# Kernel tuning notes

Hardware: AMD Instinct MI355X
Metric: run time of the kernel (lower is better)

Reference implementation:

```python
import jax, jax.numpy as jnp
import numpy as np

BATCH, NUM_BSS, NUM_USERS, M, N = 32, 8, 32, 128, 4
LAGR_ITERS = 8
PSEUDOINV_SVAL_THRESH = 1e-12


def herm(a):
    return 0.5 * (a + jnp.swapaxes(a, -1, -2).conj())


def setup_inputs() -> dict:
    key = jax.random.key(0)
    ks = jax.random.split(key, 7)
    v_re = jax.random.normal(ks[0], (BATCH, NUM_USERS, M, N), jnp.float32)
    v_im = jax.random.normal(ks[1], (BATCH, NUM_USERS, M, N), jnp.float32)
    H_re = jax.random.normal(ks[2], (NUM_BSS, NUM_USERS, N, M), jnp.float32)
    H_im = jax.random.normal(ks[3], (NUM_BSS, NUM_USERS, N, M), jnp.float32)
    noise_pow = jax.random.uniform(ks[4], (BATCH, NUM_USERS), jnp.float32, 0.05, 1.0)
    rweights = jax.random.uniform(ks[5], (BATCH, NUM_USERS), jnp.float32, 0.1, 1.0)
    bss_pow = jnp.ones((BATCH, NUM_BSS), jnp.float32)
    assign = jax.random.randint(ks[6], (NUM_USERS,), 0, NUM_BSS).astype(jnp.int32)
    return {"v_re": v_re, "v_im": v_im, "H_re": H_re, "H_im": H_im,
            "noise_pow": noise_pow, "rweights": rweights, "bss_pow": bss_pow,
            "assign": assign}


def reference(v_re, v_im, H_re, H_im, noise_pow, rweights, bss_pow, assign):
    V = v_re + 1j * v_im          # [B,K,M,N] precoders
    H = H_re + 1j * H_im          # [C,K,N,M] channel BS c -> user k
    K = V.shape[1]
    C = H.shape[0]
    Ndim = V.shape[-1]
    eyeN = jnp.eye(Ndim, dtype=V.dtype)

    # Hg[j, i] = channel from assigned-BS-of-user-j to user i
    Hg = H[assign]                                    # [K,K,N,M]
    # downlink covariance per user i: noise*I + sum_j (H[bs_j,i] V_j)(.)^H
    HV = jnp.einsum('jinm,bjmp->bijnp', Hg, V)        # [B,Ki,Kj,N,N]
    cov = jnp.einsum('bijnp,bijqp->binq', HV, HV.conj())
    cov = herm(cov + noise_pow[..., None, None] * eyeN)
    icov = herm(jnp.linalg.inv(cov))                  # [B,K,N,N]

    idx = jnp.arange(K)
    Hd = Hg[idx, idx]                                 # [K,N,M] direct channels
    HdV = jnp.einsum('knm,bkmp->bknp', Hd, V)         # [B,K,N,N]
    u = jnp.einsum('bknq,bkqp->bknp', icov, HdV)      # receive filters
    w_inv = herm(eyeN - jnp.einsum('bkqn,bkqp->bknp', u.conj(), HdV))
    w = herm(jnp.linalg.inv(w_inv))                   # MSE weights (w_poly=None)
    uwu = herm(jnp.einsum('bknp,bkpq,bkrq->bknr', u, w, u.conj()))
    # v_tilde = H_ii^H u w * rate_weight
    vt = jnp.einsum('knm,bknp,bkpq->bkmq', Hd.conj(), u, w) * rweights[..., None, None]

    # uplink covariance per BS c: sum_k rw_k * H[c,k]^H uwu_k H[c,k]
    ul = herm(jnp.einsum('cknm,bkno,ckop,bk->bcmp', H.conj(), uwu, H, rweights))

    # aux per BS: sum over assigned users of v_tilde v_tilde^H
    Q = jnp.einsum('bkmn,bkpn->bkmp', vt, vt.conj())  # [B,K,M,M]
    aux = jnp.moveaxis(
        jax.ops.segment_sum(jnp.moveaxis(Q, 1, 0), assign, num_segments=C), 0, 1)  # [B,C,M,M]

    lam, E = jnp.linalg.eigh(ul)                      # [B,C,M], [B,C,M,M]
    lam = jnp.maximum(lam, 0.0)
    c = jnp.maximum(jnp.einsum('bcmi,bcmp,bcpi->bci', E.conj(), aux, E).real, 0.0)
    c = c / bss_pow[..., None]

    # solve sum_i c_i/(lam_i+mu)^2 = 1 for mu >= 0 by bisection in [0, sqrt(sum c)]
    hi = jnp.sqrt(jnp.sum(c, -1))
    lo = jnp.zeros_like(hi)
    for _ in range(LAGR_ITERS):
        mid = 0.5 * (lo + hi)
        f = jnp.sum(c / jnp.square(lam + mid[..., None] + 1e-20), -1)
        gt = f > 1.0
        lo = jnp.where(gt, mid, lo)
        hi = jnp.where(gt, hi, mid)
    mu = jnp.maximum(0.5 * (lo + hi), 0.0)            # [B,C]

    # pseudo-inverse of loaded UL covariance via its eigendecomposition
    lam_l = lam + mu[..., None]
    lam_l = jnp.where(lam_l < PSEUDOINV_SVAL_THRESH, 1e12, lam_l)
    inv_aug = herm(jnp.einsum('bcmi,bci,bcni->bcmn', E, 1.0 / lam_l, E.conj()))

    # v update: v_k = inv_aug[assign_k] @ v_tilde_k
    v_out = jnp.einsum('bkmp,bkpn->bkmn', inv_aug[:, assign], vt)  # [B,K,M,N]
    return v_out
```

## Files before the change

kernel.cpp:

```cpp
#include <hip/hip_runtime.h>

#define B_ 32
#define C_ 8
#define K_ 32

__device__ __forceinline__ float2 cmul(float2 a, float2 b) {
  return make_float2(a.x*b.x - a.y*b.y, a.x*b.y + a.y*b.x);
}
__device__ __forceinline__ float2 cmulc(float2 a, float2 b) {
  return make_float2(a.x*b.x + a.y*b.y, a.y*b.x - a.x*b.y);
}
__device__ __forceinline__ float2 cadd(float2 a, float2 b){ return make_float2(a.x+b.x, a.y+b.y); }
__device__ __forceinline__ float2 csub(float2 a, float2 b){ return make_float2(a.x-b.x, a.y-b.y); }
__device__ __forceinline__ int SK(int r){ return r + ((r >> 3) << 1); }

__device__ void herm4_inv(float2 a[4][4], float2 out[4][4]) {
  float idg[4];
  for (int j = 0; j < 4; ++j) {
    float d = sqrtf(fmaxf(a[j][j].x, 1e-30f));
    float id = 1.f / d;
    idg[j] = id;
    a[j][j] = make_float2(d, 0.f);
    for (int r = j+1; r < 4; ++r) { a[r][j].x *= id; a[r][j].y *= id; }
    for (int c = j+1; c < 4; ++c)
      for (int r = c; r < 4; ++r)
        a[r][c] = csub(a[r][c], cmulc(a[r][j], a[c][j]));
  }
  float2 li[4][4];
  for (int j = 0; j < 4; ++j) {
    li[j][j] = make_float2(idg[j], 0.f);
    for (int r = j+1; r < 4; ++r) {
      float2 s = make_float2(0.f, 0.f);
      for (int d = j; d < r; ++d) s = cadd(s, cmul(a[r][d], li[d][j]));
      li[r][j] = make_float2(-s.x*idg[r], -s.y*idg[r]);
    }
  }
  for (int p = 0; p < 4; ++p)
    for (int q = 0; q < 4; ++q) {
      float2 s = make_float2(0.f, 0.f);
      for (int d = (p > q ? p : q); d < 4; ++d)
        s = cadd(s, cmulc(li[d][q], li[d][p]));
      out[p][q] = s;
    }
}

__global__ __launch_bounds__(512, 2) void k_fused(
    const float* __restrict__ v_re, const float* __restrict__ v_im,
    const float* __restrict__ H_re, const float* __restrict__ H_im,
    const float* __restrict__ noise_pow, const float* __restrict__ rweights,
    const float* __restrict__ bss_pow, const int* __restrict__ assign_g,
    void* __restrict__ outp, int omode)
{
  const int t = threadIdx.x;
  const int lane = t & 63, wid = t >> 6;
  const int blk = blockIdx.x;
  const int b = blk >> 3, c = blk & 7;
  const int tm = t >> 4, tp = t & 15;
  const int rbase = tm * 4, cbase = tp * 8;

  __shared__ __align__(16) float2 Arena[4160];
  __shared__ __align__(16) float2 pS[1024];
  __shared__ __align__(16) float2 dBS2[256];
  __shared__ __align__(16) float2 vS[128];
  __shared__ __align__(16) float2 wS[160];
  __shared__ __align__(16) float2 colS[160];
  __shared__ __align__(16) float2 pvS[128];
  __shared__ __align__(16) float2 tauS[128];
  __shared__ float dS[128], eS[128], cpS[128];
  __shared__ float red[8];
  __shared__ int asg[K_], ulist[K_], nc_s;

  float2* Wall = pS;
  float2* uwS  = pS + 512;
  float2* Vs   = Arena;
  float2* Tb   = Arena + 776;
  float2* covS = Arena + 1288;
  float2* HdVS = Arena + 1800;
  float2* Hs   = Arena;
  float2* Ys   = Arena + 520;
  float2* Pd   = Arena;
  float2* Bs   = Arena;

  if (t < K_) asg[t] = assign_g[t];
  if (t == 0) {
    int n2 = 0;
    for (int k = 0; k < K_; ++k) if (assign_g[k] == c) ulist[n2++] = k;
    nc_s = n2;
  }
  {
    const int k = t >> 4, n = (t >> 2) & 3, q = t & 3;
    covS[t] = make_float2((n == q) ? noise_pow[b*K_ + k] : 0.f, 0.f);
  }
  __syncthreads();
  const int nc = nc_s;
  if (nc == 0) return;
  const int cols = 4 * nc;
  const int qmax = (cols + 15) >> 4;
  const int passes = (cols + 31) >> 5;

  {
    const int pn = t >> 2;
    const int qt = t & 3;
    const int kk = pn >> 2, nn = pn & 3;
    const float2* Vq = Vs + qt*2;
    for (int j = 0; j < K_; ++j) {
      const int vb = (b*K_ + j) * 512;
      Vs[(t >> 2)*6 + (t & 3) + (t >> 7)*2] = make_float2(v_re[vb + t], v_im[vb + t]);
      __syncthreads();
      const int hb = ((asg[j]*K_ + kk)*4 + nn) * 128;
      float2 a0 = {0,0}, a1 = {0,0}, a2 = {0,0}, a3 = {0,0};
      for (int m4 = qt*32; m4 < qt*32 + 32; m4 += 4) {
        const float4 hre = *(const float4*)&H_re[hb + m4];
        const float4 him = *(const float4*)&H_im[hb + m4];
        const float hx[4] = {hre.x, hre.y, hre.z, hre.w};
        const float hy[4] = {him.x, him.y, him.z, him.w};
        #pragma unroll
        for (int i = 0; i < 4; ++i) {
          const float4 v01 = *(const float4*)&Vq[(m4 + i)*6];
          const float4 v23 = *(const float4*)&Vq[(m4 + i)*6 + 2];
          a0.x += hx[i]*v01.x - hy[i]*v01.y; a0.y += hx[i]*v01.y + hy[i]*v01.x;
          a1.x += hx[i]*v01.z - hy[i]*v01.w; a1.y += hx[i]*v01.w + hy[i]*v01.z;
          a2.x += hx[i]*v23.x - hy[i]*v23.y; a2.y += hx[i]*v23.y + hy[i]*v23.x;
          a3.x += hx[i]*v23.z - hy[i]*v23.w; a3.y += hx[i]*v23.w + hy[i]*v23.z;
        }
      }
      #pragma unroll
      for (int o = 1; o <= 2; o <<= 1) {
        a0.x += __shfl_xor(a0.x, o, 64); a0.y += __shfl_xor(a0.y, o, 64);
        a1.x += __shfl_xor(a1.x, o, 64); a1.y += __shfl_xor(a1.y, o, 64);
        a2.x += __shfl_xor(a2.x, o, 64); a2.y += __shfl_xor(a2.y, o, 64);
        a3.x += __shfl_xor(a3.x, o, 64); a3.y += __shfl_xor(a3.y, o, 64);
      }
      if (qt == 0) {
        Tb[pn*4 + 0] = a0; Tb[pn*4 + 1] = a1; Tb[pn*4 + 2] = a2; Tb[pn*4 + 3] = a3;
      }
      __syncthreads();
      {
        const int k2 = t >> 4, n2 = (t >> 2) & 3, q2 = t & 3;
        float2 acc = covS[t];
        #pragma unroll
        for (int p = 0; p < 4; ++p)
          acc = cadd(acc, cmulc(Tb[(k2*4 + n2)*4 + p], Tb[(k2*4 + q2)*4 + p]));
        covS[t] = acc;
        if (k2 == j) HdVS[k2*16 + n2*4 + q2] = Tb[(k2*4 + n2)*4 + q2];
      }
      __syncthreads();
    }
  }

  if (t < K_) {
    const int k = t;
    float2 a[4][4], ic[4][4], hv[4][4], u[4][4], wi[4][4], w[4][4], uw[4][4], W[4][4];
    const float rwk = rweights[b*K_ + k];
    for (int r = 0; r < 4; ++r)
      for (int c2 = 0; c2 < 4; ++c2) a[r][c2] = covS[k*16 + r*4 + c2];
    herm4_inv(a, ic);
    for (int r = 0; r < 4; ++r)
      for (int c2 = 0; c2 < 4; ++c2) hv[r][c2] = HdVS[k*16 + r*4 + c2];
    for (int n = 0; n < 4; ++n)
      for (int p = 0; p < 4; ++p) {
        float2 s = {0,0};
        for (int q = 0; q < 4; ++q) s = cadd(s, cmul(ic[n][q], hv[q][p]));
        u[n][p] = s;
      }
    for (int n = 0; n < 4; ++n)
      for (int p = 0; p < 4; ++p) {
        float2 s = make_float2((n == p) ? 1.f : 0.f, 0.f);
        for (int q = 0; q < 4; ++q) s = csub(s, cmulc(hv[q][p], u[q][n]));
        wi[n][p] = s;
      }
    herm4_inv(wi, w);
    for (int n = 0; n < 4; ++n)
      for (int q = 0; q < 4; ++q) {
        float2 s = {0,0};
        for (int p = 0; p < 4; ++p) s = cadd(s, cmul(u[n][p], w[p][q]));
        uw[n][q] = s;
      }
    for (int n = 0; n < 4; ++n)
      for (int r = 0; r < 4; ++r) {
        float2 s = {0,0};
        for (int q = 0; q < 4; ++q) s = cadd(s, cmulc(uw[n][q], u[r][q]));
        W[n][r] = make_float2(s.x * rwk, s.y * rwk);
      }
    for (int n = 0; n < 4; ++n)
      for (int r = n; r < 4; ++r) {
        float2 x1 = W[n][r], x2 = W[r][n];
        float2 hm = make_float2(0.5f*(x1.x + x2.x), 0.5f*(x1.y - x2.y));
        W[n][r] = hm; W[r][n] = make_float2(hm.x, -hm.y);
      }
    for (int idx = 0; idx < 16; ++idx) {
      uwS[k*16 + idx]  = uw[idx >> 2][idx & 3];
      Wall[k*16 + idx] = W[idx >> 2][idx & 3];
    }
  }
  __syncthreads();

  float2 Bv[4][8];
  #pragma unroll
  for (int j = 0; j < 4; ++j)
    #pragma unroll
    for (int q = 0; q < 8; ++q) Bv[j][q] = make_float2(0.f, 0.f);
  float trp = 0.f;
  #pragma unroll
  for (int q = 0; q < 8; ++q) {
    const int col = tp + 16*q;
    const int slot = col >> 2, qn = col & 3;
    if (slot < nc) {
      const int k = ulist[slot];
      const float rwk = rweights[b*K_ + k];
      const int hb = (c*K_ + k) * 512;
      float2 acc0 = {0,0}, acc1 = {0,0}, acc2 = {0,0}, acc3 = {0,0};
      #pragma unroll
      for (int n = 0; n < 4; ++n) {
        const float2 uwv = uwS[k*16 + n*4 + qn];
        const float4 hre = *(const float4*)&H_re[hb + n*128 + rbase];
        const float4 him = *(const float4*)&H_im[hb + n*128 + rbase];
        acc0 = cadd(acc0, cmulc(uwv, make_float2(hre.x, him.x)));
        acc1 = cadd(acc1, cmulc(uwv, make_float2(hre.y, him.y)));
        acc2 = cadd(acc2, cmulc(uwv, make_float2(hre.z, him.z)));
        acc3 = cadd(acc3, cmulc(uwv, make_float2(hre.w, him.w)));
      }
      acc0.x *= rwk; acc0.y *= rwk; acc1.x *= rwk; acc1.y *= rwk;
      acc2.x *= rwk; acc2.y *= rwk; acc3.x *= rwk; acc3.y *= rwk;
      Bv[0][q] = acc0; Bv[1][q] = acc1; Bv[2][q] = acc2; Bv[3][q] = acc3;
      trp += acc0.x*acc0.x + acc0.y*acc0.y + acc1.x*acc1.x + acc1.y*acc1.y
           + acc2.x*acc2.x + acc2.y*acc2.y + acc3.x*acc3.x + acc3.y*acc3.y;
    }
  }
  #pragma unroll
  for (int o = 32; o >= 1; o >>= 1) trp += __shfl_xor(trp, o, 64);
  if (lane == 0) red[wid] = trp;
  __syncthreads();
  const float inv_bss = 1.f / bss_pow[b*C_ + c];
  float hi = sqrtf((red[0] + red[1] + red[2] + red[3] +
                    red[4] + red[5] + red[6] + red[7]) * inv_bss);
  float lo = 0.f;

  float2 Areg[4][8];
  #pragma unroll
  for (int j = 0; j < 4; ++j)
    #pragma unroll
    for (int cc = 0; cc < 8; ++cc) Areg[j][cc] = make_float2(0.f, 0.f);
  __syncthreads();
  for (int k = 0; k < K_; ++k) {
    const int hb = (c*K_ + k) * 512;
    Hs[(t >> 7)*130 + (t & 127)] = make_float2(H_re[hb + t], H_im[hb + t]);
    __syncthreads();
    {
      const int n = t >> 7, p = t & 127;
      float2 y = {0,0};
      #pragma unroll
      for (int o = 0; o < 4; ++o) y = cadd(y, cmul(Wall[k*16 + n*4 + o], Hs[o*130 + p]));
      Ys[n*160 + p + ((p >> 3) << 1)] = y;
    }
    __syncthreads();
    #pragma unroll
    for (int n = 0; n < 4; ++n) {
      float2 h[4], y[8];
      {
        const float4 ha = *(const float4*)&Hs[n*130 + rbase];
        const float4 hc = *(const float4*)&Hs[n*130 + rbase + 2];
        h[0] = make_float2(ha.x, ha.y); h[1] = make_float2(ha.z, ha.w);
        h[2] = make_float2(hc.x, hc.y); h[3] = make_float2(hc.z, hc.w);
        const float2* yb = &Ys[n*160 + tp*10];
        #pragma unroll
        for (int a2 = 0; a2 < 8; a2 += 2) {
          const float4 y4 = *(const float4*)&yb[a2];
          y[a2] = make_float2(y4.x, y4.y); y[a2+1] = make_float2(y4.z, y4.w);
        }
      }
      #pragma unroll
      for (int j = 0; j < 4; ++j)
        #pragma unroll
        for (int cc = 0; cc < 8; ++cc) {
          Areg[j][cc].x += h[j].x*y[cc].x + h[j].y*y[cc].y;
          Areg[j][cc].y += h[j].x*y[cc].y - h[j].y*y[cc].x;
        }
    }
    __syncthreads();
  }

  if (tp == 0) {
    #pragma unroll
    for (int j = 0; j < 4; ++j) colS[SK(rbase + j)] = Areg[j][0];
  }
  __syncthreads();

  #pragma unroll 1
  for (int i = 0; i < 127; ++i) {
    float2 vr[4], vc[8], tau, sc;
    {
      const float2 x0 = colS[SK(lane)], x1 = colS[SK(lane + 64)];
      float sig = 0.f;
      if (lane >= i + 2)      sig += x0.x*x0.x + x0.y*x0.y;
      if (lane + 64 >= i + 2) sig += x1.x*x1.x + x1.y*x1.y;
      #pragma unroll
      for (int o = 32; o >= 1; o >>= 1) sig += __shfl_xor(sig, o, 64);
      const float2 al = colS[SK(i + 1)];
      float beta;
      if (sig <= 1e-30f && fabsf(al.y) <= 1e-30f) {
        beta = al.x; tau = make_float2(0.f, 0.f); sc = make_float2(0.f, 0.f);
      } else {
        const float mag = sqrtf(al.x*al.x + al.y*al.y + sig);
        beta = (al.x >= 0.f) ? -mag : mag;
        const float ib = 1.f / beta;
        tau = make_float2((beta - al.x) * ib, -al.y * ib);
        const float dx = al.x - beta, dy = al.y;
        const float dn = 1.f / (dx*dx + dy*dy);
        sc = make_float2(dx*dn, -dy*dn);
      }
      if (t == 0) { eS[i] = beta; tauS[i] = tau; }
      #pragma unroll
      for (int j = 0; j < 4; ++j) {
        const int r = rbase + j;
        const float2 x = colS[SK(r)];
        vr[j] = (r <= i) ? make_float2(0.f, 0.f)
              : (r == i + 1 ? make_float2(1.f, 0.f) : cmul(x, sc));
      }
      {
        const int cb = SK(cbase);
        const float4 c01 = *(const float4*)&colS[cb];
        const float4 c23 = *(const float4*)&colS[cb + 2];
        const float4 c45 = *(const float4*)&colS[cb + 4];
        const float4 c67 = *(const float4*)&colS[cb + 6];
        const float2 cx[8] = { make_float2(c01.x,c01.y), make_float2(c01.z,c01.w),
                               make_float2(c23.x,c23.y), make_float2(c23.z,c23.w),
                               make_float2(c45.x,c45.y), make_float2(c45.z,c45.w),
                               make_float2(c67.x,c67.y), make_float2(c67.z,c67.w) };
        #pragma unroll
        for (int cc = 0; cc < 8; ++cc) {
          const int r = cbase + cc;
          vc[cc] = (r <= i) ? make_float2(0.f, 0.f)
                 : (r == i + 1 ? make_float2(1.f, 0.f) : cmul(cx[cc], sc));
        }
      }
    }
    {
      float2 part[4];
      #pragma unroll
      for (int j = 0; j < 4; ++j) {
        float2 s = cmul(Areg[j][0], vc[0]);
        #pragma unroll
        for (int cc = 1; cc < 8; ++cc) s = cadd(s, cmul(Areg[j][cc], vc[cc]));
        part[j] = s;
      }
      #pragma unroll
      for (int o = 1; o <= 8; o <<= 1) {
        #pragma unroll
        for (int j = 0; j < 4; ++j) {
          part[j].x += __shfl_xor(part[j].x, o, 64);
          part[j].y += __shfl_xor(part[j].y, o, 64);
        }
      }
      #pragma unroll
      for (int j = 0; j < 4; ++j) if (tp == j) pvS[rbase + j] = part[j];
      #pragma unroll
      for (int q = 0; q < 8; ++q) {
        if (q >= qmax) continue;
        float2 s = {0.f, 0.f};
        #pragma unroll
        for (int j = 0; j < 4; ++j) s = cadd(s, cmulc(Bv[j][q], vr[j]));
        Pd[tm*130 + tp + 16*q] = s;
      }
    }
    __syncthreads();

    if (wid == 0) {
      float2 p0 = {0.f,0.f}, p1 = {0.f,0.f};
      if (lane > i)      p0 = cmul(tau, pvS[lane]);
      if (lane + 64 > i) p1 = cmul(tau, pvS[lane + 64]);
      float2 v0, v1;
      v0 = (lane <= i) ? make_float2(0.f,0.f)
         : (lane == i + 1 ? make_float2(1.f,0.f) : cmul(colS[SK(lane)], sc));
      { const int r1 = lane + 64;
        v1 = (r1 <= i) ? make_float2(0.f,0.f)
           : (r1 == i + 1 ? make_float2(1.f,0.f) : cmul(colS[SK(r1)], sc)); }
      float2 d0 = cadd(cmulc(p0, v0), cmulc(p1, v1));
      #pragma unroll
      for (int o = 32; o >= 1; o >>= 1) {
        d0.x += __shfl_xor(d0.x, o, 64);
        d0.y += __shfl_xor(d0.y, o, 64);
      }
      const float alr = -0.5f * (tau.x*d0.x + tau.y*d0.y);
      wS[SK(lane)]      = cadd(p0, make_float2(alr*v0.x, alr*v0.y));
      wS[SK(lane + 64)] = cadd(p1, make_float2(alr*v1.x, alr*v1.y));
    } else if (t < 320) {
      const int col = (t - 64) & 127;
      const int half = (t - 64) >> 7;
      float2 s = {0.f, 0.f};
      #pragma unroll
      for (int g = 0; g < 16; ++g) s = cadd(s, Pd[(half*16 + g)*130 + col]);
      dBS2[half*128 + col] = s;
    }
    __syncthreads();

    {
      float2 wr[4], wc[8];
      #pragma unroll
      for (int j = 0; j < 4; ++j) wr[j] = wS[SK(rbase + j)];
      {
        const int cb = SK(cbase);
        const float4 w01 = *(const float4*)&wS[cb];
        const float4 w23 = *(const float4*)&wS[cb + 2];
        const float4 w45 = *(const float4*)&wS[cb + 4];
        const float4 w67 = *(const float4*)&wS[cb + 6];
        wc[0] = make_float2(w01.x,w01.y); wc[1] = make_float2(w01.z,w01.w);
        wc[2] = make_float2(w23.x,w23.y); wc[3] = make_float2(w23.z,w23.w);
        wc[4] = make_float2(w45.x,w45.y); wc[5] = make_float2(w45.z,w45.w);
        wc[6] = make_float2(w67.x,w67.y); wc[7] = make_float2(w67.z,w67.w);
      }
      #pragma unroll
      for (int j = 0; j < 4; ++j)
        #pragma unroll
        for (int cc = 0; cc < 8; ++cc)
          Areg[j][cc] = csub(Areg[j][cc], cadd(cmulc(vr[j], wc[cc]), cmulc(wr[j], vc[cc])));
      const float2 tauc = make_float2(tau.x, -tau.y);
      #pragma unroll
      for (int q = 0; q < 8; ++q) {
        if (q >= qmax) continue;
        const float2 dBt = cmul(tauc, cadd(dBS2[tp + 16*q], dBS2[128 + tp + 16*q]));
        #pragma unroll
        for (int j = 0; j < 4; ++j) Bv[j][q] = csub(Bv[j][q], cmul(dBt, vr[j]));
      }
      if (tp == (i >> 3)) {
        #pragma unroll
        for (int cc = 0; cc < 8; ++cc) if (cc == (i & 7)) {
          #pragma unroll
          for (int j = 0; j < 4; ++j) if (rbase + j >= i + 1) Areg[j][cc] = vr[j];
        }
      }
      if (tp == ((i + 1) >> 3)) {
        #pragma unroll
        for (int cc = 0; cc < 8; ++cc) if (cc == ((i + 1) & 7)) {
          #pragma unroll
          for (int j = 0; j < 4; ++j) colS[SK(rbase + j)] = Areg[j][cc];
        }
      }
    }
    __syncthreads();
  }

  if (tp == (tm >> 1)) {
    const int co = (tm & 1) * 4;
    #pragma unroll
    for (int j = 0; j < 4; ++j)
      #pragma unroll
      for (int cc = 0; cc < 8; ++cc)
        if (cc == co + j) dS[rbase + j] = Areg[j][cc].x;
  }
  __syncthreads();

  for (int it = 0; it <= 8; ++it) {
    const float mu = 0.5f * (lo + hi);
    float fsum = 0.f;
    #pragma unroll
    for (int p = 0; p < 4; ++p) {
      if (p >= passes) continue;
      __syncthreads();
      #pragma unroll
      for (int j = 0; j < 4; ++j) {
        Bs[(rbase + j)*32 + tp]      = Bv[j][2*p];
        Bs[(rbase + j)*32 + tp + 16] = Bv[j][2*p + 1];
      }
      __syncthreads();
      if (wid == 0) {
        const int colg = 32*p + lane;
        const bool act = (lane < 32) && (colg < cols);
        float m = dS[0] + mu;
        float im = 1.f / m;
        float2 g = act ? Bs[lane] : make_float2(0.f, 0.f);
        g.x *= im; g.y *= im;
        if (act) Bs[lane] = g;
        float cp = eS[0] * im;
        if (lane == 0) cpS[0] = cp;
        for (int r = 1; r < 128; ++r) {
          const float e0 = eS[r-1];
          m = dS[r] + mu - e0 * cp;
          im = 1.f / m;
          float2 gr = act ? Bs[r*32 + lane] : make_float2(0.f, 0.f);
          gr.x = (gr.x - e0 * g.x) * im;
          gr.y = (gr.y - e0 * g.y) * im;
          g = gr;
          if (act) Bs[r*32 + lane] = gr;
          if (r < 127) { cp = eS[r] * im; if (lane == 0) cpS[r] = cp; }
        }
        float2 z = g;
        float acc = z.x*z.x + z.y*z.y;
        for (int r = 126; r >= 0; --r) {
          const float cpr = cpS[r];
          const float2 gp = act ? Bs[r*32 + lane] : make_float2(0.f, 0.f);
          z.x = gp.x - cpr * z.x;
          z.y = gp.y - cpr * z.y;
          acc += z.x*z.x + z.y*z.y;
          if (it == 8 && act) Bs[r*32 + lane] = z;
        }
        if (act) fsum += acc;
      }
      if (it == 8) {
        __syncthreads();
        #pragma unroll
        for (int j = 0; j < 4; ++j) {
          Bv[j][2*p]     = Bs[(rbase + j)*32 + tp];
          Bv[j][2*p + 1] = Bs[(rbase + j)*32 + tp + 16];
        }
      }
    }
    if (it < 8 && wid == 0) {
      #pragma unroll
      for (int o = 32; o >= 1; o >>= 1) fsum += __shfl_xor(fsum, o, 64);
      const float f = fsum * inv_bss;
      if (f > 1.0f) lo = mu; else hi = mu;
    }
  }
  __syncthreads();

  #pragma unroll 1
  for (int i = 126; i >= 0; --i) {
    if (t < 128 && t <= i) vS[t] = make_float2(0.f, 0.f);
    if (tp == (i >> 3)) {
      #pragma unroll
      for (int cc = 0; cc < 8; ++cc) if (cc == (i & 7)) {
        #pragma unroll
        for (int j = 0; j < 4; ++j) if (rbase + j >= i + 1) vS[rbase + j] = Areg[j][cc];
      }
    }
    __syncthreads();
    float2 vr[4];
    #pragma unroll
    for (int j = 0; j < 4; ++j) vr[j] = vS[rbase + j];
    #pragma unroll
    for (int q = 0; q < 8; ++q) {
      if (q >= qmax) continue;
      float2 s = {0.f, 0.f};
      #pragma unroll
      for (int j = 0; j < 4; ++j) s = cadd(s, cmulc(Bv[j][q], vr[j]));
      Pd[tm*130 + tp + 16*q] = s;
    }
    __syncthreads();
    if (t < 256) {
      const int col = t & 127;
      const int half = t >> 7;
      float2 s = {0.f, 0.f};
      #pragma unroll
      for (int g = 0; g < 16; ++g) s = cadd(s, Pd[(half*16 + g)*130 + col]);
      dBS2[half*128 + col] = s;
    }
    __syncthreads();
    {
      const float2 tau2 = tauS[i];
      #pragma unroll
      for (int q = 0; q < 8; ++q) {
        if (q >= qmax) continue;
        const float2 dBt = cmul(tau2, cadd(dBS2[tp + 16*q], dBS2[128 + tp + 16*q]));
        #pragma unroll
        for (int j = 0; j < 4; ++j) Bv[j][q] = csub(Bv[j][q], cmul(dBt, vr[j]));
      }
    }
  }

  #pragma unroll
  for (int q = 0; q < 8; ++q) {
    const int col = tp + 16*q;
    const int slot = col >> 2, qn = col & 3;
    if (slot < nc) {
      const int k = ulist[slot];
      const size_t base = (size_t)(b*K_ + k) * 512;
      #pragma unroll
      for (int j = 0; j < 4; ++j) {
        const size_t oe = base + (size_t)(rbase + j)*4 + qn;
        if (omode == 0) ((float2*)outp)[oe] = Bv[j][q];
        else            ((float*)outp)[oe]  = Bv[j][q].x;
      }
    }
  }
}

extern "C" void kernel_launch(void* const* d_in, const int* in_sizes, int n_in,
                              void* d_out, int out_size, void* d_ws, size_t ws_size,
                              hipStream_t stream)
{
  (void)in_sizes; (void)n_in; (void)d_ws; (void)ws_size;
  const float* v_re   = (const float*)d_in[0];
  const float* v_im   = (const float*)d_in[1];
  const float* H_re   = (const float*)d_in[2];
  const float* H_im   = (const float*)d_in[3];
  const float* noise  = (const float*)d_in[4];
  const float* rw     = (const float*)d_in[5];
  const float* bss    = (const float*)d_in[6];
  const int*   assign = (const int*)d_in[7];

  const int omode = (out_size == B_*K_*128*4) ? 1 : 0;

  hipLaunchKernelGGL(k_fused, dim3(B_*C_), dim3(512), 0, stream,
                     v_re, v_im, H_re, H_im, noise, rw, bss, assign, d_out, omode);
}
```

Baseline: 1.337 ms.

## Batch Householder reflector application to RHS in blocks of sixteen via shared memory

Moves the right-hand-side matrix out of registers into a padded shared-memory buffer. Instead of applying each Householder reflector to it inside the per-step tridiagonalization loop, the reflectors are stored in groups of 16 and applied per column by warps using shuffle reductions. The same blocked scheme replaces the per-step back-transformation loop. The tridiagonal solves now run directly on shared columns in a single warp, and the covariance accumulation processes two users per synchronization. Shared memory grows sharply and launch bounds drop to one block per CU, which trades occupancy for fewer barriers.

```diff
diff --git a/kernel.cpp b/kernel.cpp
--- a/kernel.cpp
+++ b/kernel.cpp
@@ -3,6 +3,8 @@
 #define B_ 32
 #define C_ 8
 #define K_ 32
+#define NCMAX 96
+#define BSTR 129
 
 __device__ __forceinline__ float2 cmul(float2 a, float2 b) {
   return make_float2(a.x*b.x - a.y*b.y, a.x*b.y + a.y*b.x);
@@ -44,7 +46,7 @@
     }
 }
 
-__global__ __launch_bounds__(512, 2) void k_fused(
+__global__ __launch_bounds__(512, 1) void k_fused(
     const float* __restrict__ v_re, const float* __restrict__ v_im,
     const float* __restrict__ H_re, const float* __restrict__ H_im,
     const float* __restrict__ noise_pow, const float* __restrict__ rweights,
@@ -58,13 +60,12 @@
   const int tm = t >> 4, tp = t & 15;
   const int rbase = tm * 4, cbase = tp * 8;
 
-  __shared__ __align__(16) float2 Arena[4160];
+  __shared__ __align__(16) float2 Bs[NCMAX * BSTR];
+  __shared__ __align__(16) float2 Arena[4224];
+  __shared__ __align__(16) float2 Vp[16 * 128];
   __shared__ __align__(16) float2 pS[1024];
-  __shared__ __align__(16) float2 dBS2[256];
-  __shared__ __align__(16) float2 vS[128];
-  __shared__ __align__(16) float2 wS[160];
   __shared__ __align__(16) float2 colS[160];
-  __shared__ __align__(16) float2 pvS[128];
+  __shared__ __align__(16) float2 pvS[160];
   __shared__ __align__(16) float2 tauS[128];
   __shared__ float dS[128], eS[128], cpS[128];
   __shared__ float red[8];
@@ -72,14 +73,11 @@
 
   float2* Wall = pS;
   float2* uwS  = pS + 512;
-  float2* Vs   = Arena;
-  float2* Tb   = Arena + 776;
-  float2* covS = Arena + 1288;
-  float2* HdVS = Arena + 1800;
+  float2* covS = Arena + 2576;
+  float2* HdVS = Arena + 3088;
   float2* Hs   = Arena;
   float2* Ys   = Arena + 520;
-  float2* Pd   = Arena;
-  float2* Bs   = Arena;
+  float2* Tsc  = Arena;
 
   if (t < K_) asg[t] = assign_g[t];
   if (t == 0) {
@@ -95,44 +93,60 @@
   const int nc = nc_s;
   if (nc == 0) return;
   const int cols = 4 * nc;
-  const int qmax = (cols + 15) >> 4;
   const int passes = (cols + 31) >> 5;
 
   {
-    const int pn = t >> 2;
-    const int qt = t & 3;
+    const int pn = t >> 2, qt = t & 3;
     const int kk = pn >> 2, nn = pn & 3;
-    const float2* Vq = Vs + qt*2;
-    for (int j = 0; j < K_; ++j) {
-      const int vb = (b*K_ + j) * 512;
-      Vs[(t >> 2)*6 + (t & 3) + (t >> 7)*2] = make_float2(v_re[vb + t], v_im[vb + t]);
+    float2* Tb0 = Arena + 1552;
+    float2* Tb1 = Arena + 2064;
+    for (int j = 0; j < K_; j += 2) {
+      #pragma unroll
+      for (int bf = 0; bf < 2; ++bf) {
+        const int vb = (b*K_ + j + bf) * 512;
+        Arena[bf*776 + (t >> 2)*6 + (t & 3) + (t >> 7)*2] =
+            make_float2(v_re[vb + t], v_im[vb + t]);
+      }
       __syncthreads();
-      const int hb = ((asg[j]*K_ + kk)*4 + nn) * 128;
-      float2 a0 = {0,0}, a1 = {0,0}, a2 = {0,0}, a3 = {0,0};
-      for (int m4 = qt*32; m4 < qt*32 + 32; m4 += 4) {
-        const float4 hre = *(const float4*)&H_re[hb + m4];
-        const float4 him = *(const float4*)&H_im[hb + m4];
-        const float hx[4] = {hre.x, hre.y, hre.z, hre.w};
-        const float hy[4] = {him.x, him.y, him.z, him.w};
-        #pragma unroll
-        for (int i = 0; i < 4; ++i) {
-          const float4 v01 = *(const float4*)&Vq[(m4 + i)*6];
-          const float4 v23 = *(const float4*)&Vq[(m4 + i)*6 + 2];
-          a0.x += hx[i]*v01.x - hy[i]*v01.y; a0.y += hx[i]*v01.y + hy[i]*v01.x;
-          a1.x += hx[i]*v01.z - hy[i]*v01.w; a1.y += hx[i]*v01.w + hy[i]*v01.z;
-          a2.x += hx[i]*v23.x - hy[i]*v23.y; a2.y += hx[i]*v23.y + hy[i]*v23.x;
-          a3.x += hx[i]*v23.z - hy[i]*v23.w; a3.y += hx[i]*v23.w + hy[i]*v23.z;
-        }
+      float2 rr[2][4];
+      #pragma unroll
+      for (int bf = 0; bf < 2; ++bf) {
+        const float2* Vq = Arena + bf*776 + qt*2;
+        const int hb = ((asg[j + bf]*K_ + kk)*4 + nn) * 128;
+        float2 a0 = {0,0}, a1 = {0,0}, a2 = {0,0}, a3 = {0,0};
+        for (int m4 = qt*32; m4 < qt*32 + 32; m4 += 4) {
+          const float4 hre = *(const float4*)&H_re[hb + m4];
+          const float4 him = *(const float4*)&H_im[hb + m4];
+          const float hx[4] = {hre.x, hre.y, hre.z, hre.w};
+          const float hy[4] = {him.x, him.y, him.z, him.w};
+          #pragma unroll
+          for (int i2 = 0; i2 < 4; ++i2) {
+            const float4 v01 = *(const float4*)&Vq[(m4 + i2)*6];
+            const float4 v23 = *(const float4*)&Vq[(m4 + i2)*6 + 2];
+            a0.x += hx[i2]*v01.x - hy[i2]*v01.y; a0.y += hx[i2]*v01.y + hy[i2]*v01.x;
+            a1.x += hx[i2]*v01.z - hy[i2]*v01.w; a1.y += hx[i2]*v01.w + hy[i2]*v01.z;
+            a2.x += hx[i2]*v23.x - hy[i2]*v23.y; a2.y += hx[i2]*v23.y + hy[i2]*v23.x;
+            a3.x += hx[i2]*v23.z - hy[i2]*v23.w; a3.y += hx[i2]*v23.w + hy[i2]*v23.z;
+          }
+        }
+        rr[bf][0] = a0; rr[bf][1] = a1; rr[bf][2] = a2; rr[bf][3] = a3;
       }
       #pragma unroll
       for (int o = 1; o <= 2; o <<= 1) {
-        a0.x += __shfl_xor(a0.x, o, 64); a0.y += __shfl_xor(a0.y, o, 64);
-        a1.x += __shfl_xor(a1.x, o, 64); a1.y += __shfl_xor(a1.y, o, 64);
-        a2.x += __shfl_xor(a2.x, o, 64); a2.y += __shfl_xor(a2.y, o, 64);
-        a3.x += __shfl_xor(a3.x, o, 64); a3.y += __shfl_xor(a3.y, o, 64);
+        #pragma unroll
+        for (int bf = 0; bf < 2; ++bf)
+          #pragma unroll
+          for (int p = 0; p < 4; ++p) {
+            rr[bf][p].x += __shfl_xor(rr[bf][p].x, o, 64);
+            rr[bf][p].y += __shfl_xor(rr[bf][p].y, o, 64);
+          }
       }
       if (qt == 0) {
-        Tb[pn*4 + 0] = a0; Tb[pn*4 + 1] = a1; Tb[pn*4 + 2] = a2; Tb[pn*4 + 3] = a3;
+        #pragma unroll
+        for (int p = 0; p < 4; ++p) {
+          Tb0[pn*4 + p] = rr[0][p];
+          Tb1[pn*4 + p] = rr[1][p];
+        }
       }
       __syncthreads();
       {
@@ -140,9 +154,13 @@
         float2 acc = covS[t];
         #pragma unroll
         for (int p = 0; p < 4; ++p)
-          acc = cadd(acc, cmulc(Tb[(k2*4 + n2)*4 + p], Tb[(k2*4 + q2)*4 + p]));
+          acc = cadd(acc, cmulc(Tb0[(k2*4 + n2)*4 + p], Tb0[(k2*4 + q2)*4 + p]));
+        #pragma unroll
+        for (int p = 0; p < 4; ++p)
+          acc = cadd(acc, cmulc(Tb1[(k2*4 + n2)*4 + p], Tb1[(k2*4 + q2)*4 + p]));
         covS[t] = acc;
-        if (k2 == j) HdVS[k2*16 + n2*4 + q2] = Tb[(k2*4 + n2)*4 + q2];
+        if (k2 == j)     HdVS[k2*16 + n2*4 + q2] = Tb0[(k2*4 + n2)*4 + q2];
+        if (k2 == j + 1) HdVS[k2*16 + n2*4 + q2] = Tb1[(k2*4 + n2)*4 + q2];
       }
       __syncthreads();
     }
@@ -195,11 +213,6 @@
   }
   __syncthreads();
 
-  float2 Bv[4][8];
-  #pragma unroll
-  for (int j = 0; j < 4; ++j)
-    #pragma unroll
-    for (int q = 0; q < 8; ++q) Bv[j][q] = make_float2(0.f, 0.f);
   float trp = 0.f;
   #pragma unroll
   for (int q = 0; q < 8; ++q) {
@@ -222,7 +235,10 @@
       }
       acc0.x *= rwk; acc0.y *= rwk; acc1.x *= rwk; acc1.y *= rwk;
       acc2.x *= rwk; acc2.y *= rwk; acc3.x *= rwk; acc3.y *= rwk;
-      Bv[0][q] = acc0; Bv[1][q] = acc1; Bv[2][q] = acc2; Bv[3][q] = acc3;
+      Bs[col*BSTR + rbase]     = acc0;
+      Bs[col*BSTR + rbase + 1] = acc1;
+      Bs[col*BSTR + rbase + 2] = acc2;
+      Bs[col*BSTR + rbase + 3] = acc3;
       trp += acc0.x*acc0.x + acc0.y*acc0.y + acc1.x*acc1.x + acc1.y*acc1.y
            + acc2.x*acc2.x + acc2.y*acc2.y + acc3.x*acc3.x + acc3.y*acc3.y;
     }
@@ -289,6 +305,7 @@
   #pragma unroll 1
   for (int i = 0; i < 127; ++i) {
     float2 vr[4], vc[8], tau, sc;
+    const int slot = (i & 15) << 7;
     {
       const float2 x0 = colS[SK(lane)], x1 = colS[SK(lane + 64)];
       float sig = 0.f;
@@ -334,8 +351,10 @@
                  : (r == i + 1 ? make_float2(1.f, 0.f) : cmul(cx[cc], sc));
         }
       }
-    }
-    {
+      if (tp == 0) {
+        #pragma unroll
+        for (int j = 0; j < 4; ++j) Vp[slot + rbase + j] = vr[j];
+      }
       float2 part[4];
       #pragma unroll
       for (int j = 0; j < 4; ++j) {
@@ -353,28 +372,16 @@
         }
       }
       #pragma unroll
-      for (int j = 0; j < 4; ++j) if (tp == j) pvS[rbase + j] = part[j];
-      #pragma unroll
-      for (int q = 0; q < 8; ++q) {
-        if (q >= qmax) continue;
-        float2 s = {0.f, 0.f};
-        #pragma unroll
-        for (int j = 0; j < 4; ++j) s = cadd(s, cmulc(Bv[j][q], vr[j]));
-        Pd[tm*130 + tp + 16*q] = s;
-      }
+      for (int j = 0; j < 4; ++j) if (tp == j) pvS[SK(rbase + j)] = part[j];
     }
     __syncthreads();
 
-    if (wid == 0) {
-      float2 p0 = {0.f,0.f}, p1 = {0.f,0.f};
-      if (lane > i)      p0 = cmul(tau, pvS[lane]);
-      if (lane + 64 > i) p1 = cmul(tau, pvS[lane + 64]);
-      float2 v0, v1;
-      v0 = (lane <= i) ? make_float2(0.f,0.f)
-         : (lane == i + 1 ? make_float2(1.f,0.f) : cmul(colS[SK(lane)], sc));
-      { const int r1 = lane + 64;
-        v1 = (r1 <= i) ? make_float2(0.f,0.f)
-           : (r1 == i + 1 ? make_float2(1.f,0.f) : cmul(colS[SK(r1)], sc)); }
+    {
+      float2 p0 = make_float2(0.f, 0.f), p1 = make_float2(0.f, 0.f);
+      if (lane > i)      p0 = cmul(tau, pvS[SK(lane)]);
+      if (lane + 64 > i) p1 = cmul(tau, pvS[SK(lane + 64)]);
+      const float2 v0 = Vp[slot + lane];
+      const float2 v1 = Vp[slot + lane + 64];
       float2 d0 = cadd(cmulc(p0, v0), cmulc(p1, v1));
       #pragma unroll
       for (int o = 32; o >= 1; o >>= 1) {
@@ -382,194 +389,224 @@
         d0.y += __shfl_xor(d0.y, o, 64);
       }
       const float alr = -0.5f * (tau.x*d0.x + tau.y*d0.y);
-      wS[SK(lane)]      = cadd(p0, make_float2(alr*v0.x, alr*v0.y));
-      wS[SK(lane + 64)] = cadd(p1, make_float2(alr*v1.x, alr*v1.y));
-    } else if (t < 320) {
-      const int col = (t - 64) & 127;
-      const int half = (t - 64) >> 7;
-      float2 s = {0.f, 0.f};
-      #pragma unroll
-      for (int g = 0; g < 16; ++g) s = cadd(s, Pd[(half*16 + g)*130 + col]);
-      dBS2[half*128 + col] = s;
+      float2 wr[4];
+      #pragma unroll
+      for (int j = 0; j < 4; ++j) {
+        const int r = rbase + j;
+        float2 p = (r > i) ? cmul(tau, pvS[SK(r)]) : make_float2(0.f, 0.f);
+        wr[j] = make_float2(p.x + alr*vr[j].x, p.y + alr*vr[j].y);
+      }
+      #pragma unroll
+      for (int cc = 0; cc < 8; ++cc) {
+        const int r = cbase + cc;
+        float2 p = (r > i) ? cmul(tau, pvS[SK(r)]) : make_float2(0.f, 0.f);
+        const float2 wcv = make_float2(p.x + alr*vc[cc].x, p.y + alr*vc[cc].y);
+        #pragma unroll
+        for (int j = 0; j < 4; ++j)
+          Areg[j][cc] = csub(Areg[j][cc], cadd(cmulc(vr[j], wcv), cmulc(wr[j], vc[cc])));
+      }
+      if (tp == (i >> 3)) {
+        #pragma unroll
+        for (int cc = 0; cc < 8; ++cc) if (cc == (i & 7)) {
+          #pragma unroll
+          for (int j = 0; j < 4; ++j) if (rbase + j >= i + 1) Areg[j][cc] = vr[j];
+        }
+      }
+      if (tp == ((i + 1) >> 3)) {
+        #pragma unroll
+        for (int cc = 0; cc < 8; ++cc) if (cc == ((i + 1) & 7)) {
+          #pragma unroll
+          for (int j = 0; j < 4; ++j) colS[SK(rbase + j)] = Areg[j][cc];
+        }
+      }
     }
     __syncthreads();
 
-    {
-      float2 wr[4], wc[8];
-      #pragma unroll
-      for (int j = 0; j < 4; ++j) wr[j] = wS[SK(rbase + j)];
-      {
-        const int cb = SK(cbase);
-        const float4 w01 = *(const float4*)&wS[cb];
-        const float4 w23 = *(const float4*)&wS[cb + 2];
-        const float4 w45 = *(const float4*)&wS[cb + 4];
-        const float4 w67 = *(const float4*)&wS[cb + 6];
-        wc[0] = make_float2(w01.x,w01.y); wc[1] = make_float2(w01.z,w01.w);
-        wc[2] = make_float2(w23.x,w23.y); wc[3] = make_float2(w23.z,w23.w);
-        wc[4] = make_float2(w45.x,w45.y); wc[5] = make_float2(w45.z,w45.w);
-        wc[6] = make_float2(w67.x,w67.y); wc[7] = make_float2(w67.z,w67.w);
-      }
-      #pragma unroll
-      for (int j = 0; j < 4; ++j)
-        #pragma unroll
-        for (int cc = 0; cc < 8; ++cc)
-          Areg[j][cc] = csub(Areg[j][cc], cadd(cmulc(vr[j], wc[cc]), cmulc(wr[j], vc[cc])));
-      const float2 tauc = make_float2(tau.x, -tau.y);
-      #pragma unroll
-      for (int q = 0; q < 8; ++q) {
-        if (q >= qmax) continue;
-        const float2 dBt = cmul(tauc, cadd(dBS2[tp + 16*q], dBS2[128 + tp + 16*q]));
-        #pragma unroll
-        for (int j = 0; j < 4; ++j) Bv[j][q] = csub(Bv[j][q], cmul(dBt, vr[j]));
-      }
-      if (tp == (i >> 3)) {
-        #pragma unroll
-        for (int cc = 0; cc < 8; ++cc) if (cc == (i & 7)) {
-          #pragma unroll
-          for (int j = 0; j < 4; ++j) if (rbase + j >= i + 1) Areg[j][cc] = vr[j];
-        }
-      }
-      if (tp == ((i + 1) >> 3)) {
-        #pragma unroll
-        for (int cc = 0; cc < 8; ++cc) if (cc == ((i + 1) & 7)) {
-          #pragma unroll
-          for (int j = 0; j < 4; ++j) colS[SK(rbase + j)] = Areg[j][cc];
-        }
-      }
-    }
-    __syncthreads();
-  }
-
-  if (tp == (tm >> 1)) {
-    const int co = (tm & 1) * 4;
-    #pragma unroll
-    for (int j = 0; j < 4; ++j)
-      #pragma unroll
-      for (int cc = 0; cc < 8; ++cc)
-        if (cc == co + j) dS[rbase + j] = Areg[j][cc].x;
+    if ((i & 15) == 15 || i == 126) {
+      const int p0i = i & ~15;
+      const int smax = i - p0i;
+      for (int base = 0; base < cols; base += 32) {
+        float2 z0[4], z1[4];
+        bool act[4];
+        #pragma unroll
+        for (int qq = 0; qq < 4; ++qq) {
+          const int col = base + wid + 8*qq;
+          act[qq] = (col < cols);
+          const int cc2 = act[qq] ? col : 0;
+          z0[qq] = Bs[cc2*BSTR + lane];
+          z1[qq] = Bs[cc2*BSTR + lane + 64];
+        }
+        for (int s = 0; s <= smax; ++s) {
+          const float2 tv = tauS[p0i + s];
+          const float2 tc = make_float2(tv.x, -tv.y);
+          const float2 v0 = Vp[(s << 7) + lane];
+          const float2 v1 = Vp[(s << 7) + lane + 64];
+          float2 d[4];
+          #pragma unroll
+          for (int qq = 0; qq < 4; ++qq)
+            d[qq] = cadd(cmulc(z0[qq], v0), cmulc(z1[qq], v1));
+          #pragma unroll
+          for (int o = 32; o >= 1; o >>= 1) {
+            #pragma unroll
+            for (int qq = 0; qq < 4; ++qq) {
+              d[qq].x += __shfl_xor(d[qq].x, o, 64);
+              d[qq].y += __shfl_xor(d[qq].y, o, 64);
+            }
+          }
+          #pragma unroll
+          for (int qq = 0; qq < 4; ++qq) {
+            const float2 td = cmul(tc, d[qq]);
+            z0[qq] = csub(z0[qq], cmul(td, v0));
+            z1[qq] = csub(z1[qq], cmul(td, v1));
+          }
+        }
+        #pragma unroll
+        for (int qq = 0; qq < 4; ++qq) if (act[qq]) {
+          const int col = base + wid + 8*qq;
+          Bs[col*BSTR + lane]      = z0[qq];
+          Bs[col*BSTR + lane + 64] = z1[qq];
+        }
+      }
+      __syncthreads();
+    }
+  }
+
+  #pragma unroll
+  for (int j = 0; j < 4; ++j) {
+    const int r = rbase + j;
+    if (tp == (r >> 3)) {
+      #pragma unroll
+      for (int cc = 0; cc < 8; ++cc) if (cc == (r & 7)) dS[r] = Areg[j][cc].x;
+    }
   }
   __syncthreads();
 
-  for (int it = 0; it <= 8; ++it) {
-    const float mu = 0.5f * (lo + hi);
-    float fsum = 0.f;
-    #pragma unroll
-    for (int p = 0; p < 4; ++p) {
-      if (p >= passes) continue;
-      __syncthreads();
-      #pragma unroll
-      for (int j = 0; j < 4; ++j) {
-        Bs[(rbase + j)*32 + tp]      = Bv[j][2*p];
-        Bs[(rbase + j)*32 + tp + 16] = Bv[j][2*p + 1];
-      }
-      __syncthreads();
-      if (wid == 0) {
-        const int colg = 32*p + lane;
+  if (wid == 0) {
+    for (int it = 0; it <= 8; ++it) {
+      const float mu = 0.5f * (lo + hi);
+      float fsum = 0.f;
+      for (int p = 0; p < passes; ++p) {
+        const int colg = 32*p + (lane & 31);
         const bool act = (lane < 32) && (colg < cols);
+        float2* Bcol = Bs + colg*BSTR;
         float m = dS[0] + mu;
         float im = 1.f / m;
-        float2 g = act ? Bs[lane] : make_float2(0.f, 0.f);
+        float2 g = act ? Bcol[0] : make_float2(0.f, 0.f);
         g.x *= im; g.y *= im;
-        if (act) Bs[lane] = g;
+        if (act) Tsc[lane] = g;
         float cp = eS[0] * im;
         if (lane == 0) cpS[0] = cp;
         for (int r = 1; r < 128; ++r) {
           const float e0 = eS[r-1];
           m = dS[r] + mu - e0 * cp;
           im = 1.f / m;
-          float2 gr = act ? Bs[r*32 + lane] : make_float2(0.f, 0.f);
+          float2 gr = act ? Bcol[r] : make_float2(0.f, 0.f);
           gr.x = (gr.x - e0 * g.x) * im;
           gr.y = (gr.y - e0 * g.y) * im;
           g = gr;
-          if (act) Bs[r*32 + lane] = gr;
+          if (act) Tsc[r*33 + lane] = gr;
           if (r < 127) { cp = eS[r] * im; if (lane == 0) cpS[r] = cp; }
         }
         float2 z = g;
         float acc = z.x*z.x + z.y*z.y;
+        if (it == 8 && act) Bcol[127] = z;
         for (int r = 126; r >= 0; --r) {
           const float cpr = cpS[r];
-          const float2 gp = act ? Bs[r*32 + lane] : make_float2(0.f, 0.f);
+          const float2 gp = act ? Tsc[r*33 + lane] : make_float2(0.f, 0.f);
           z.x = gp.x - cpr * z.x;
           z.y = gp.y - cpr * z.y;
           acc += z.x*z.x + z.y*z.y;
-          if (it == 8 && act) Bs[r*32 + lane] = z;
+          if (it == 8 && act) Bcol[r] = z;
         }
         if (act) fsum += acc;
       }
-      if (it == 8) {
-        __syncthreads();
-        #pragma unroll
-        for (int j = 0; j < 4; ++j) {
-          Bv[j][2*p]     = Bs[(rbase + j)*32 + tp];
-          Bv[j][2*p + 1] = Bs[(rbase + j)*32 + tp + 16];
-        }
-      }
-    }
-    if (it < 8 && wid == 0) {
-      #pragma unroll
-      for (int o = 32; o >= 1; o >>= 1) fsum += __shfl_xor(fsum, o, 64);
-      const float f = fsum * inv_bss;
-      if (f > 1.0f) lo = mu; else hi = mu;
+      if (it < 8) {
+        #pragma unroll
+        for (int o = 32; o >= 1; o >>= 1) fsum += __shfl_xor(fsum, o, 64);
+        const float f = fsum * inv_bss;
+        if (f > 1.0f) lo = mu; else hi = mu;
+      }
     }
   }
   __syncthreads();
 
-  #pragma unroll 1
-  for (int i = 126; i >= 0; --i) {
-    if (t < 128 && t <= i) vS[t] = make_float2(0.f, 0.f);
-    if (tp == (i >> 3)) {
-      #pragma unroll
-      for (int cc = 0; cc < 8; ++cc) if (cc == (i & 7)) {
-        #pragma unroll
-        for (int j = 0; j < 4; ++j) if (rbase + j >= i + 1) vS[rbase + j] = Areg[j][cc];
-      }
-    }
-    __syncthreads();
-    float2 vr[4];
+  for (int base = 0; base < cols; base += 32) {
+    float2 z0[4], z1[4];
+    bool act[4];
     #pragma unroll
-    for (int j = 0; j < 4; ++j) vr[j] = vS[rbase + j];
+    for (int qq = 0; qq < 4; ++qq) {
+      const int col = base + wid + 8*qq;
+      act[qq] = (col < cols);
+      const int cc2 = act[qq] ? col : 0;
+      z0[qq] = Bs[cc2*BSTR + lane];
+      z1[qq] = Bs[cc2*BSTR + lane + 64];
+    }
+    for (int P = 7; P >= 0; --P) {
+      const int p0i = P * 16;
+      const int smax = (P == 7) ? 14 : 15;
+      __syncthreads();
+      if (tp == 2*P) {
+        #pragma unroll
+        for (int s = 0; s < 8; ++s) {
+          const int ii = p0i + s;
+          #pragma unroll
+          for (int j = 0; j < 4; ++j) {
+            const int r = rbase + j;
+            Vp[(s << 7) + r] = (r >= ii + 1) ? Areg[j][s] : make_float2(0.f, 0.f);
+          }
+        }
+      }
+      if (tp == 2*P + 1) {
+        #pragma unroll
+        for (int s = 8; s < 16; ++s) {
+          if (s > smax) continue;
+          const int ii = p0i + s;
+          #pragma unroll
+          for (int j = 0; j < 4; ++j) {
+            const int r = rbase + j;
+            Vp[(s << 7) + r] = (r >= ii + 1) ? Areg[j][s - 8] : make_float2(0.f, 0.f);
+          }
+        }
+      }
+      __syncthreads();
+      for (int s = smax; s >= 0; --s) {
+        const float2 tv = tauS[p0i + s];
+        const float2 v0 = Vp[(s << 7) + lane];
+        const float2 v1 = Vp[(s << 7) + lane + 64];
+        float2 d[4];
+        #pragma unroll
+        for (int qq = 0; qq < 4; ++qq)
+          d[qq] = cadd(cmulc(z0[qq], v0), cmulc(z1[qq], v1));
+        #pragma unroll
+        for (int o = 32; o >= 1; o >>= 1) {
+          #pragma unroll
+          for (int qq = 0; qq < 4; ++qq) {
+            d[qq].x += __shfl_xor(d[qq].x, o, 64);
+            d[qq].y += __shfl_xor(d[qq].y, o, 64);
+          }
+        }
+        #pragma unroll
+        for (int qq = 0; qq < 4; ++qq) {
+          const float2 td = cmul(tv, d[qq]);
+          z0[qq] = csub(z0[qq], cmul(td, v0));
+          z1[qq] = csub(z1[qq], cmul(td, v1));
+        }
+      }
+    }
     #pragma unroll
-    for (int q = 0; q < 8; ++q) {
-      if (q >= qmax) continue;
-      float2 s = {0.f, 0.f};
-      #pragma unroll
-      for (int j = 0; j < 4; ++j) s = cadd(s, cmulc(Bv[j][q], vr[j]));
-      Pd[tm*130 + tp + 16*q] = s;
-    }
-    __syncthreads();
-    if (t < 256) {
-      const int col = t & 127;
-      const int half = t >> 7;
-      float2 s = {0.f, 0.f};
-      #pragma unroll
-      for (int g = 0; g < 16; ++g) s = cadd(s, Pd[(half*16 + g)*130 + col]);
-      dBS2[half*128 + col] = s;
-    }
-    __syncthreads();
-    {
-      const float2 tau2 = tauS[i];
-      #pragma unroll
-      for (int q = 0; q < 8; ++q) {
-        if (q >= qmax) continue;
-        const float2 dBt = cmul(tau2, cadd(dBS2[tp + 16*q], dBS2[128 + tp + 16*q]));
-        #pragma unroll
-        for (int j = 0; j < 4; ++j) Bv[j][q] = csub(Bv[j][q], cmul(dBt, vr[j]));
-      }
-    }
-  }
-
-  #pragma unroll
-  for (int q = 0; q < 8; ++q) {
-    const int col = tp + 16*q;
-    const int slot = col >> 2, qn = col & 3;
-    if (slot < nc) {
-      const int k = ulist[slot];
-      const size_t base = (size_t)(b*K_ + k) * 512;
-      #pragma unroll
-      for (int j = 0; j < 4; ++j) {
-        const size_t oe = base + (size_t)(rbase + j)*4 + qn;
-        if (omode == 0) ((float2*)outp)[oe] = Bv[j][q];
-        else            ((float*)outp)[oe]  = Bv[j][q].x;
+    for (int qq = 0; qq < 4; ++qq) if (act[qq]) {
+      const int col = base + wid + 8*qq;
+      const int slotc = col >> 2, qn = col & 3;
+      const int k = ulist[slotc];
+      const size_t obase = (size_t)(b*K_ + k) * 512;
+      const size_t oe0 = obase + (size_t)lane*4 + qn;
+      const size_t oe1 = obase + (size_t)(lane + 64)*4 + qn;
+      if (omode == 0) {
+        ((float2*)outp)[oe0] = z0[qq];
+        ((float2*)outp)[oe1] = z1[qq];
+      } else {
+        ((float*)outp)[oe0] = z0[qq].x;
+        ((float*)outp)[oe1] = z1[qq].x;
       }
     }
   }
```

Result: slower. 1.472 ms (+10.1%).
